# Optimization experiments

Measured on AMD Instinct MI355X. Metric: run time of the kernel, lower is better.

## Reference

```python
import jax, jax.numpy as jnp
import numpy as np

N = 50000      # nodes
E = 1600000    # edges (avg degree 32)
F_IN = 256     # input feature dim
H = 128        # hidden == output size of GCN
C = 40         # num_class


def setup_inputs() -> dict:
    key = jax.random.key(0)
    ks = jax.random.split(key, 13)
    inp = {
        "features": jax.random.normal(ks[0], (N, F_IN), dtype=jnp.float32),
        "src": jax.random.randint(ks[1], (E,), 0, N, dtype=jnp.int32),
        "dst": jax.random.randint(ks[2], (E,), 0, N, dtype=jnp.int32),
        "edge_weight": jax.random.uniform(ks[3], (E,), dtype=jnp.float32),
        "y": jax.random.normal(ks[4], (N, C), dtype=jnp.float32),
        # GCN layer 1
        "W1": jax.random.normal(ks[5], (F_IN, H), dtype=jnp.float32) / np.sqrt(F_IN),
        "b1": jnp.zeros((H,), dtype=jnp.float32),
        # GCN layer 2
        "W2": jax.random.normal(ks[6], (H, H), dtype=jnp.float32) / np.sqrt(H),
        "b2": jnp.zeros((H,), dtype=jnp.float32),
        # y_fc_emb: Linear(num_class, output_size)
        "We": jax.random.normal(ks[7], (C, H), dtype=jnp.float32) / np.sqrt(C),
        "be": jnp.zeros((H,), dtype=jnp.float32),
        # y_fc: Linear(hidden*2, num_class)
        "Wf": jax.random.normal(ks[8], (2 * H, C), dtype=jnp.float32) / np.sqrt(2 * H),
        "bf": jnp.zeros((C,), dtype=jnp.float32),
    }
    return inp


def _spmm(edge_weight, src, dst, x, n):
    # (sparse adj) @ x : out[i] = sum_{(j->i)} w_ji * x[j]
    return jax.ops.segment_sum(edge_weight[:, None] * x[src], dst, num_segments=n)


def reference(features, src, dst, edge_weight, y, W1, b1, W2, b2, We, be, Wf, bf):
    n = features.shape[0]
    # F.normalize: L2 row-normalize with eps=1e-12 clamp
    norm = jnp.maximum(jnp.linalg.norm(features, axis=1, keepdims=True), 1e-12)
    x = features / norm
    # GCN layer 1: relu(adj @ (x @ W1) + b1)   (dropout = 0)
    h = jax.nn.relu(_spmm(edge_weight, src, dst, x @ W1, n) + b1)
    # GCN layer 2: adj @ (h @ W2) + b2
    h = _spmm(edge_weight, src, dst, h @ W2, n) + b2
    # label embedding + head
    y_emb = y @ We + be
    logits = jnp.concatenate([y_emb, h], axis=1) @ Wf + bf
    return jax.nn.softmax(logits, axis=-1)
```

## Files before the change

### kernel.cpp

```cpp
#include <hip/hip_runtime.h>
#include <hip/hip_bf16.h>
#include <hip/hip_fp16.h>
#include <cstdint>
#include <cstddef>
#include <cmath>

#define F_IN 256
#define HDIM 128
#define CCLS 40
#define NBMAX 1024
#define EPB_H 16384

typedef short bf16x8 __attribute__((ext_vector_type(8)));
typedef float f32x4 __attribute__((ext_vector_type(4)));

__device__ inline unsigned pkbf(float a, float b) {
  __hip_bfloat162 h = __float22bfloat162_rn(make_float2(a, b));
  unsigned u;
  __builtin_memcpy(&u, &h, 4);
  return u;
}
__device__ inline unsigned short bfr(float f) {
  __hip_bfloat16 h = __float2bfloat16(f);
  unsigned short u;
  __builtin_memcpy(&u, &h, 2);
  return u;
}
__device__ inline float f16tof(unsigned short hb) {
  __half hv;
  __builtin_memcpy(&hv, &hb, 2);
  return __half2float(hv);
}
__device__ inline unsigned short ftof16(float f) {
  __half hv = __float2half(f);
  unsigned short u;
  __builtin_memcpy(&u, &hv, 2);
  return u;
}

__global__ __launch_bounds__(256) void prep_kernel(const float* __restrict__ x,
                                                   unsigned short* __restrict__ featbf,
                                                   const float* __restrict__ W1,
                                                   const float* __restrict__ W2,
                                                   unsigned short* __restrict__ W1T,
                                                   unsigned short* __restrict__ W2T,
                                                   const float* __restrict__ We,
                                                   const float* __restrict__ be,
                                                   const float* __restrict__ Wf,
                                                   const float* __restrict__ bf,
                                                   float* __restrict__ Wc,
                                                   float* __restrict__ bc,
                                                   const int* __restrict__ dst,
                                                   int* __restrict__ gcount,
                                                   int n, int e, int nb) {
  const int b = blockIdx.x;
  const int t = threadIdx.x;
  const int nblk = (n + 15) >> 4;
  if (b < nblk) {
    const int wv = t >> 6, l = t & 63;
    const int r0 = b * 16 + wv * 4;
    const bool q0 = r0 < n, q1 = r0 + 1 < n, q2 = r0 + 2 < n, q3 = r0 + 3 < n;
    const float* p = x + (size_t)r0 * F_IN + l * 4;
    float4 z = make_float4(0.f, 0.f, 0.f, 0.f);
    float4 v0 = q0 ? *(const float4*)(p) : z;
    float4 v1 = q1 ? *(const float4*)(p + F_IN) : z;
    float4 v2 = q2 ? *(const float4*)(p + 2 * F_IN) : z;
    float4 v3 = q3 ? *(const float4*)(p + 3 * F_IN) : z;
    float s0 = v0.x * v0.x + v0.y * v0.y + v0.z * v0.z + v0.w * v0.w;
    float s1 = v1.x * v1.x + v1.y * v1.y + v1.z * v1.z + v1.w * v1.w;
    float s2 = v2.x * v2.x + v2.y * v2.y + v2.z * v2.z + v2.w * v2.w;
    float s3 = v3.x * v3.x + v3.y * v3.y + v3.z * v3.z + v3.w * v3.w;
#pragma unroll
    for (int off = 32; off; off >>= 1) {
      s0 += __shfl_xor(s0, off, 64);
      s1 += __shfl_xor(s1, off, 64);
      s2 += __shfl_xor(s2, off, 64);
      s3 += __shfl_xor(s3, off, 64);
    }
    float i0 = 1.0f / fmaxf(sqrtf(s0), 1e-12f);
    float i1 = 1.0f / fmaxf(sqrtf(s1), 1e-12f);
    float i2 = 1.0f / fmaxf(sqrtf(s2), 1e-12f);
    float i3 = 1.0f / fmaxf(sqrtf(s3), 1e-12f);
    unsigned short* o = featbf + (size_t)r0 * F_IN + l * 4;
    if (q0) *(uint2*)(o) = make_uint2(pkbf(v0.x * i0, v0.y * i0), pkbf(v0.z * i0, v0.w * i0));
    if (q1) *(uint2*)(o + F_IN) = make_uint2(pkbf(v1.x * i1, v1.y * i1), pkbf(v1.z * i1, v1.w * i1));
    if (q2) *(uint2*)(o + 2 * F_IN) = make_uint2(pkbf(v2.x * i2, v2.y * i2), pkbf(v2.z * i2, v2.w * i2));
    if (q3) *(uint2*)(o + 3 * F_IN) = make_uint2(pkbf(v3.x * i3, v3.y * i3), pkbf(v3.z * i3, v3.w * i3));
  } else if (b < nblk + 192) {
    int idx = (b - nblk) * 256 + t;
    if (idx < 128 * 256) {
      int nr = idx >> 8, k = idx & 255;
      W1T[idx] = bfr(W1[k * 128 + nr]);
    } else {
      int i2 = idx - 128 * 256;
      if (i2 < 128 * 128) {
        int nr = i2 >> 7, k = i2 & 127;
        W2T[i2] = bfr(W2[k * 128 + nr]);
      }
    }
  } else if (b < nblk + 194) {
    int part = b - (nblk + 192);
    int lo = part * 800, hi = lo + 800;
    for (int i = lo + t; i < hi; i += 256) {
      int c = i / CCLS, j = i % CCLS;
      float s = 0.f;
      for (int f = 0; f < HDIM; ++f) s += We[c * HDIM + f] * Wf[f * CCLS + j];
      Wc[i] = s;
    }
    if (part == 0 && t < CCLS) {
      float s = bf[t];
      for (int f = 0; f < HDIM; ++f) s += be[f] * Wf[f * CCLS + t];
      bc[t] = s;
    }
  } else {
    __shared__ int h[NBMAX];
    for (int i = t; i < nb; i += 256) h[i] = 0;
    __syncthreads();
    int b4 = (b - (nblk + 194)) * (EPB_H / 4);
#pragma unroll
    for (int k = 0; k < EPB_H / 1024; ++k) {
      int gi = b4 + k * 256 + t;
      int e0 = gi * 4;
      int4 d = make_int4(-1, -1, -1, -1);
      if (e0 + 3 < e) d = ((const int4*)dst)[gi];
      else if (e0 < e) {
        d.x = dst[e0];
        if (e0 + 1 < e) d.y = dst[e0 + 1];
        if (e0 + 2 < e) d.z = dst[e0 + 2];
      }
      if (d.x >= 0) atomicAdd(&h[d.x >> 6], 1);
      if (d.y >= 0) atomicAdd(&h[d.y >> 6], 1);
      if (d.z >= 0) atomicAdd(&h[d.z >> 6], 1);
      if (d.w >= 0) atomicAdd(&h[d.w >> 6], 1);
    }
    __syncthreads();
    for (int i = t; i < nb; i += 256)
      if (h[i]) atomicAdd(&gcount[i], h[i]);
  }
}

__global__ __launch_bounds__(256) void bucket_scan(const int* __restrict__ gcount,
                                                   int* __restrict__ boff,
                                                   int* __restrict__ gcursor,
                                                   int* __restrict__ row_off,
                                                   int nb, int n) {
  __shared__ int part[256];
  int t = threadIdx.x;
  int v[4];
  int s = 0;
#pragma unroll
  for (int k = 0; k < 4; ++k) {
    int i = t * 4 + k;
    v[k] = (i < nb) ? gcount[i] : 0;
    s += v[k];
  }
  part[t] = s;
  __syncthreads();
  for (int off = 1; off < 256; off <<= 1) {
    int x = part[t];
    if (t >= off) x += part[t - off];
    __syncthreads();
    part[t] = x;
    __syncthreads();
  }
  int run = (t == 0) ? 0 : part[t - 1];
#pragma unroll
  for (int k = 0; k < 4; ++k) {
    int i = t * 4 + k;
    if (i < nb) { boff[i] = run; gcursor[i] = run; }
    run += v[k];
  }
  if (t == 255) { boff[nb] = part[255]; row_off[n] = part[255]; }
}

#define EPB 8192
__global__ __launch_bounds__(256) void bucket_scatter(const int* __restrict__ src,
                                                      const int* __restrict__ dst,
                                                      const float* __restrict__ w,
                                                      int* __restrict__ gcursor,
                                                      uint2* __restrict__ ews, int e, int nb) {
  __shared__ int hist[NBMAX];
  __shared__ int gbase[NBMAX];
  __shared__ int lcur[NBMAX];
  const int t = threadIdx.x;
  for (int i = t; i < nb; i += 256) { hist[i] = 0; lcur[i] = 0; }
  __syncthreads();
  const int b4 = blockIdx.x * 2048;
  int4 dv[8];
#pragma unroll
  for (int k = 0; k < 8; ++k) {
    int gi = b4 + k * 256 + t;
    int e0 = gi * 4;
    int4 d = make_int4(-1, -1, -1, -1);
    if (e0 + 3 < e) d = ((const int4*)dst)[gi];
    else if (e0 < e) {
      d.x = dst[e0];
      if (e0 + 1 < e) d.y = dst[e0 + 1];
      if (e0 + 2 < e) d.z = dst[e0 + 2];
    }
    dv[k] = d;
    if (d.x >= 0) atomicAdd(&hist[d.x >> 6], 1);
    if (d.y >= 0) atomicAdd(&hist[d.y >> 6], 1);
    if (d.z >= 0) atomicAdd(&hist[d.z >> 6], 1);
    if (d.w >= 0) atomicAdd(&hist[d.w >> 6], 1);
  }
  __syncthreads();
  for (int i = t; i < nb; i += 256) {
    int c = hist[i];
    gbase[i] = c ? atomicAdd(&gcursor[i], c) : 0;
  }
  __syncthreads();
#pragma unroll
  for (int k = 0; k < 8; ++k) {
    int gi = b4 + k * 256 + t;
    int e0 = gi * 4;
    if (e0 >= e) continue;
    int4 s4 = make_int4(0, 0, 0, 0);
    float4 w4 = make_float4(0.f, 0.f, 0.f, 0.f);
    if (e0 + 3 < e) { s4 = ((const int4*)src)[gi]; w4 = ((const float4*)w)[gi]; }
    else {
      s4.x = src[e0]; w4.x = w[e0];
      if (e0 + 1 < e) { s4.y = src[e0 + 1]; w4.y = w[e0 + 1]; }
      if (e0 + 2 < e) { s4.z = src[e0 + 2]; w4.z = w[e0 + 2]; }
    }
    int4 d = dv[k];
    if (d.x >= 0) { int bb = d.x >> 6; int r = atomicAdd(&lcur[bb], 1);
      ews[gbase[bb] + r] = make_uint2(((unsigned)(d.x & 63) << 26) | (unsigned)s4.x, __float_as_uint(w4.x)); }
    if (d.y >= 0) { int bb = d.y >> 6; int r = atomicAdd(&lcur[bb], 1);
      ews[gbase[bb] + r] = make_uint2(((unsigned)(d.y & 63) << 26) | (unsigned)s4.y, __float_as_uint(w4.y)); }
    if (d.z >= 0) { int bb = d.z >> 6; int r = atomicAdd(&lcur[bb], 1);
      ews[gbase[bb] + r] = make_uint2(((unsigned)(d.z & 63) << 26) | (unsigned)s4.z, __float_as_uint(w4.z)); }
    if (d.w >= 0) { int bb = d.w >> 6; int r = atomicAdd(&lcur[bb], 1);
      ews[gbase[bb] + r] = make_uint2(((unsigned)(d.w & 63) << 26) | (unsigned)s4.w, __float_as_uint(w4.w)); }
  }
}

__global__ __launch_bounds__(256) void bucket_sort(const uint2* __restrict__ ews,
                                                   const int* __restrict__ boff,
                                                   unsigned* __restrict__ ews2,
                                                   int* __restrict__ row_off,
                                                   int n) {
  __shared__ int cnt64[64];
  __shared__ int cur[64];
  const int t = threadIdx.x;
  const int b = blockIdx.x;
  const int e0 = boff[b], e1 = boff[b + 1];
  if (t < 64) cnt64[t] = 0;
  __syncthreads();
  for (int i = e0 + t; i < e1; i += 256) atomicAdd(&cnt64[(unsigned)ews[i].x >> 26], 1);
  __syncthreads();
  if (t == 0) {
    int run = 0;
    for (int d = 0; d < 64; ++d) {
      int c = cnt64[d];
      cur[d] = run;
      run += c;
    }
  }
  __syncthreads();
  if (t < 64) {
    int node = b * 64 + t;
    if (node < n) row_off[node] = e0 + cur[t];
  }
  __syncthreads();
  for (int i = e0 + t; i < e1; i += 256) {
    uint2 p = ews[i];
    int d = (unsigned)p.x >> 26;
    int pos = e0 + atomicAdd(&cur[d], 1);
    unsigned rec = (p.x & 0xFFFFu) | ((unsigned)ftof16(__uint_as_float(p.y)) << 16);
    ews2[pos] = rec;
  }
}

#define SPMM_PAIR(ua, ub)                                                      \
  {                                                                            \
    unsigned u = half ? (ub) : (ua);                                           \
    float wt = f16tof((unsigned short)(u >> 16));                              \
    const uint2 xv = *(const uint2*)(xin + (size_t)(u & 0xFFFFu) * HDIM + fo); \
    acc.x = fmaf(wt, __uint_as_float(xv.x << 16), acc.x);                      \
    acc.y = fmaf(wt, __uint_as_float(xv.x & 0xFFFF0000u), acc.y);              \
    acc.z = fmaf(wt, __uint_as_float(xv.y << 16), acc.z);                      \
    acc.w = fmaf(wt, __uint_as_float(xv.y & 0xFFFF0000u), acc.w);              \
  }

template <int OUT_BF16>
__global__ __launch_bounds__(256) void spmm_bf16(const unsigned short* __restrict__ xin,
                                                 const unsigned* __restrict__ ews,
                                                 const int* __restrict__ row_off,
                                                 const float* __restrict__ bias,
                                                 void* __restrict__ outp, int n,
                                                 int do_relu) {
  const int t = threadIdx.x;
  const int l = t & 63;
  const int node = blockIdx.x * 4 + (t >> 6);
  if (node >= n) return;
  const int ue0 = __builtin_amdgcn_readfirstlane(row_off[node]);
  const int ue1 = __builtin_amdgcn_readfirstlane(row_off[node + 1]);
  const int cnt = ue1 - ue0;
  const unsigned* ep = ews + ue0;
  const int fo = (l & 31) * 4;
  const int half = l >> 5;
  float4 acc = make_float4(0.f, 0.f, 0.f, 0.f);

  int k = 0;
  for (; k + 8 <= cnt; k += 8) {
    unsigned a0 = ep[k + 0], a1 = ep[k + 1], a2 = ep[k + 2], a3 = ep[k + 3];
    unsigned a4 = ep[k + 4], a5 = ep[k + 5], a6 = ep[k + 6], a7 = ep[k + 7];
    SPMM_PAIR(a0, a1);
    SPMM_PAIR(a2, a3);
    SPMM_PAIR(a4, a5);
    SPMM_PAIR(a6, a7);
  }
  for (; k < cnt; k += 2) {
    unsigned a0 = ep[k];
    unsigned a1 = (k + 1 < cnt) ? ep[k + 1] : 0u;
    SPMM_PAIR(a0, a1);
  }

  acc.x += __shfl_xor(acc.x, 32, 64);
  acc.y += __shfl_xor(acc.y, 32, 64);
  acc.z += __shfl_xor(acc.z, 32, 64);
  acc.w += __shfl_xor(acc.w, 32, 64);
  if (l < 32) {
    float4 bv = *(const float4*)(bias + fo);
    float4 r = make_float4(acc.x + bv.x, acc.y + bv.y, acc.z + bv.z, acc.w + bv.w);
    if (do_relu) {
      r.x = fmaxf(r.x, 0.f); r.y = fmaxf(r.y, 0.f);
      r.z = fmaxf(r.z, 0.f); r.w = fmaxf(r.w, 0.f);
    }
    if (OUT_BF16) {
      uint2 o = make_uint2(pkbf(r.x, r.y), pkbf(r.z, r.w));
      *(uint2*)((unsigned short*)outp + (size_t)node * HDIM + fo) = o;
    } else {
      *(float4*)((float*)outp + (size_t)node * HDIM + fo) = r;
    }
  }
}

template <int K>
__global__ __launch_bounds__(256) void gemm_mfma(const unsigned short* __restrict__ A,
                                                 const unsigned short* __restrict__ WT,
                                                 unsigned short* __restrict__ C, int M) {
  const int t = threadIdx.x;
  const int w = t >> 6, l = t & 63;
  const int ln = l & 15, quad = l >> 4;
  const int m0 = blockIdx.x * 64 + w * 16;
  const int arow = m0 + ln;
  const unsigned short* aptr = A + (size_t)(arow < M ? arow : (M - 1)) * K + quad * 8;

  f32x4 acc[8];
#pragma unroll
  for (int i = 0; i < 8; ++i) acc[i] = (f32x4){0.f, 0.f, 0.f, 0.f};

#pragma unroll
  for (int k0 = 0; k0 < K; k0 += 32) {
    bf16x8 af = *(const bf16x8*)(aptr + k0);
#pragma unroll
    for (int ti = 0; ti < 8; ++ti) {
      bf16x8 bf = *(const bf16x8*)(WT + (size_t)(ti * 16 + ln) * K + k0 + quad * 8);
      acc[ti] = __builtin_amdgcn_mfma_f32_16x16x32_bf16(af, bf, acc[ti], 0, 0, 0);
    }
  }

#pragma unroll
  for (int r = 0; r < 4; ++r) {
    int grow = m0 + quad * 4 + r;
    if (grow < M) {
      unsigned short* cp = C + (size_t)grow * HDIM + ln;
#pragma unroll
      for (int ti = 0; ti < 8; ++ti) cp[ti * 16] = bfr(acc[ti][r]);
    }
  }
}

__global__ __launch_bounds__(64) void head_kernel(const float* __restrict__ y,
                                                  const float* __restrict__ h2,
                                                  const float* __restrict__ Wc,
                                                  const float* __restrict__ bc,
                                                  const float* __restrict__ Wf,
                                                  float* __restrict__ out, int n) {
  __shared__ float sW[169 * CCLS];
  const int t = threadIdx.x;
  for (int i = t; i < 400; i += 64) ((float4*)sW)[i] = ((const float4*)Wc)[i];
  for (int i = t; i < 1280; i += 64)
    ((float4*)(sW + CCLS * CCLS))[i] = ((const float4*)(Wf + HDIM * CCLS))[i];
  if (t < 10) ((float4*)(sW + 168 * CCLS))[t] = ((const float4*)bc)[t];
  __syncthreads();

  const int node = blockIdx.x * 64 + t;
  const int nc = node < n ? node : n - 1;
  const float* zy = y + (size_t)nc * CCLS;
  const float* zh = h2 + (size_t)nc * HDIM;

  float acc[40];
#pragma unroll
  for (int cq = 0; cq < 10; ++cq) {
    float4 b4 = *(const float4*)&sW[168 * CCLS + cq * 4];
    acc[cq * 4 + 0] = b4.x; acc[cq * 4 + 1] = b4.y;
    acc[cq * 4 + 2] = b4.z; acc[cq * 4 + 3] = b4.w;
  }

#pragma unroll 2
  for (int kc = 0; kc < 10; ++kc) {
    float4 zv = *(const float4*)(zy + kc * 4);
    float zj[4] = {zv.x, zv.y, zv.z, zv.w};
#pragma unroll
    for (int j = 0; j < 4; ++j) {
      const float* wr = sW + (kc * 4 + j) * CCLS;
#pragma unroll
      for (int cq = 0; cq < 10; ++cq) {
        float4 w4 = *(const float4*)(wr + cq * 4);
        acc[cq * 4 + 0] = fmaf(zj[j], w4.x, acc[cq * 4 + 0]);
        acc[cq * 4 + 1] = fmaf(zj[j], w4.y, acc[cq * 4 + 1]);
        acc[cq * 4 + 2] = fmaf(zj[j], w4.z, acc[cq * 4 + 2]);
        acc[cq * 4 + 3] = fmaf(zj[j], w4.w, acc[cq * 4 + 3]);
      }
    }
  }
#pragma unroll 2
  for (int kc = 0; kc < 32; ++kc) {
    float4 zv = *(const float4*)(zh + kc * 4);
    float zj[4] = {zv.x, zv.y, zv.z, zv.w};
#pragma unroll
    for (int j = 0; j < 4; ++j) {
      const float* wr = sW + (40 + kc * 4 + j) * CCLS;
#pragma unroll
      for (int cq = 0; cq < 10; ++cq) {
        float4 w4 = *(const float4*)(wr + cq * 4);
        acc[cq * 4 + 0] = fmaf(zj[j], w4.x, acc[cq * 4 + 0]);
        acc[cq * 4 + 1] = fmaf(zj[j], w4.y, acc[cq * 4 + 1]);
        acc[cq * 4 + 2] = fmaf(zj[j], w4.z, acc[cq * 4 + 2]);
        acc[cq * 4 + 3] = fmaf(zj[j], w4.w, acc[cq * 4 + 3]);
      }
    }
  }

  float m = acc[0];
#pragma unroll
  for (int c = 1; c < 40; ++c) m = fmaxf(m, acc[c]);
  float sum = 0.f;
#pragma unroll
  for (int c = 0; c < 40; ++c) { acc[c] = __expf(acc[c] - m); sum += acc[c]; }
  float inv = 1.0f / sum;
  if (node < n) {
    float* op = out + (size_t)node * CCLS;
#pragma unroll
    for (int cq = 0; cq < 10; ++cq) {
      float4 o = make_float4(acc[cq * 4 + 0] * inv, acc[cq * 4 + 1] * inv,
                             acc[cq * 4 + 2] * inv, acc[cq * 4 + 3] * inv);
      *(float4*)(op + cq * 4) = o;
    }
  }
}

extern "C" void kernel_launch(void* const* d_in, const int* in_sizes, int n_in,
                              void* d_out, int out_size, void* d_ws, size_t ws_size,
                              hipStream_t stream) {
  (void)n_in; (void)out_size; (void)ws_size;
  const float* features = (const float*)d_in[0];
  const int*   src      = (const int*)d_in[1];
  const int*   dst      = (const int*)d_in[2];
  const float* ew       = (const float*)d_in[3];
  const float* y        = (const float*)d_in[4];
  const float* W1       = (const float*)d_in[5];
  const float* b1       = (const float*)d_in[6];
  const float* W2       = (const float*)d_in[7];
  const float* b2       = (const float*)d_in[8];
  const float* We       = (const float*)d_in[9];
  const float* be       = (const float*)d_in[10];
  const float* Wf       = (const float*)d_in[11];
  const float* bf       = (const float*)d_in[12];
  float* out = (float*)d_out;

  const int n = in_sizes[0] / F_IN;
  const int e = in_sizes[1];
  const int nb = (n + 63) >> 6;

  char* w = (char*)d_ws;
  auto take = [&](size_t bytes) {
    char* p = w;
    w += (bytes + 255) & ~(size_t)255;
    return p;
  };
  int*   gcount   = (int*)take((size_t)nb * 4);
  int*   boff     = (int*)take((size_t)(nb + 1) * 4);
  int*   gcursor  = (int*)take((size_t)nb * 4);
  int*   row_off  = (int*)take((size_t)(n + 1) * 4);
  uint2* ews      = (uint2*)take((size_t)e * 8);
  unsigned* ews2  = (unsigned*)take((size_t)(e + 16) * 4);
  unsigned short* featbf = (unsigned short*)take((size_t)n * F_IN * 2);
  unsigned short* bufH1  = (unsigned short*)take((size_t)n * HDIM * 2);
  unsigned short* bufH2  = (unsigned short*)take((size_t)n * HDIM * 2);
  float* bufS     = (float*)take((size_t)n * HDIM * 4);
  unsigned short* W1T = (unsigned short*)take((size_t)HDIM * F_IN * 2);
  unsigned short* W2T = (unsigned short*)take((size_t)HDIM * HDIM * 2);
  float* Wc       = (float*)take(CCLS * CCLS * 4);
  float* bc       = (float*)take(CCLS * 4);

  const int nblk = (n + 15) >> 4;
  const int hb = (e + EPB_H - 1) / EPB_H;
  hipMemsetAsync(gcount, 0, (size_t)nb * 4, stream);
  prep_kernel<<<nblk + 194 + hb, 256, 0, stream>>>(features, featbf, W1, W2, W1T, W2T,
                                                   We, be, Wf, bf, Wc, bc, dst, gcount,
                                                   n, e, nb);
  bucket_scan<<<1, 256, 0, stream>>>(gcount, boff, gcursor, row_off, nb, n);
  bucket_scatter<<<(e + EPB - 1) / EPB, 256, 0, stream>>>(src, dst, ew, gcursor, ews, e, nb);
  bucket_sort<<<nb, 256, 0, stream>>>(ews, boff, ews2, row_off, n);

  gemm_mfma<F_IN><<<(n + 63) / 64, 256, 0, stream>>>(featbf, W1T, bufH1, n);
  spmm_bf16<1><<<(n + 3) / 4, 256, 0, stream>>>(bufH1, ews2, row_off, b1, bufH2, n, 1);
  gemm_mfma<HDIM><<<(n + 63) / 64, 256, 0, stream>>>(bufH2, W2T, bufH1, n);
  spmm_bf16<0><<<(n + 3) / 4, 256, 0, stream>>>(bufH1, ews2, row_off, b2, bufS, n, 0);
  head_kernel<<<(n + 63) / 64, 64, 0, stream>>>(y, bufS, Wc, bc, Wf, out, n);
}
```

Measured before the change: 384.0 us.

## Split hidden features into column-chunk layout and run SpMM per chunk

Intermediate activations are stored in a chunked layout of 8 column blocks of 16 features ([chunk][node][16]). The SpMM runs eight blocks per node group, one per feature chunk, so each chunk's working set (50000 nodes × 32 bytes) is small enough to stay cache-resident while edges are gathered. The GEMM and head kernels are adapted to read and write this layout. The trade-off is that edge indices and weights are re-read eight times, and each gather becomes a 4-byte access with more shuffle reductions.

```diff
diff --git a/kernel.cpp b/kernel.cpp
--- a/kernel.cpp
+++ b/kernel.cpp
@@ -272,72 +272,66 @@
   }
 }
 
-#define SPMM_PAIR(ua, ub)                                                      \
-  {                                                                            \
-    unsigned u = half ? (ub) : (ua);                                           \
-    float wt = f16tof((unsigned short)(u >> 16));                              \
-    const uint2 xv = *(const uint2*)(xin + (size_t)(u & 0xFFFFu) * HDIM + fo); \
-    acc.x = fmaf(wt, __uint_as_float(xv.x << 16), acc.x);                      \
-    acc.y = fmaf(wt, __uint_as_float(xv.x & 0xFFFF0000u), acc.y);              \
-    acc.z = fmaf(wt, __uint_as_float(xv.y << 16), acc.z);                      \
-    acc.w = fmaf(wt, __uint_as_float(xv.y & 0xFFFF0000u), acc.w);              \
-  }
-
 template <int OUT_BF16>
-__global__ __launch_bounds__(256) void spmm_bf16(const unsigned short* __restrict__ xin,
-                                                 const unsigned* __restrict__ ews,
-                                                 const int* __restrict__ row_off,
-                                                 const float* __restrict__ bias,
-                                                 void* __restrict__ outp, int n,
-                                                 int do_relu) {
+__global__ __launch_bounds__(256) void spmm_chunk(const unsigned short* __restrict__ xin,
+                                                  const unsigned* __restrict__ ews,
+                                                  const int* __restrict__ row_off,
+                                                  const float* __restrict__ bias,
+                                                  void* __restrict__ outp, int n,
+                                                  int do_relu) {
   const int t = threadIdx.x;
   const int l = t & 63;
-  const int node = blockIdx.x * 4 + (t >> 6);
+  const int chunk = blockIdx.x & 7;
+  const int node = (blockIdx.x >> 3) * 4 + (t >> 6);
   if (node >= n) return;
   const int ue0 = __builtin_amdgcn_readfirstlane(row_off[node]);
   const int ue1 = __builtin_amdgcn_readfirstlane(row_off[node + 1]);
   const int cnt = ue1 - ue0;
   const unsigned* ep = ews + ue0;
-  const int fo = (l & 31) * 4;
-  const int half = l >> 5;
-  float4 acc = make_float4(0.f, 0.f, 0.f, 0.f);
-
+  const int g = l >> 3;
+  const int sub = l & 7;
+  const unsigned short* xc = xin + (size_t)chunk * n * 16 + sub * 2;
+  float ax = 0.f, ay = 0.f;
   int k = 0;
-  for (; k + 8 <= cnt; k += 8) {
-    unsigned a0 = ep[k + 0], a1 = ep[k + 1], a2 = ep[k + 2], a3 = ep[k + 3];
-    unsigned a4 = ep[k + 4], a5 = ep[k + 5], a6 = ep[k + 6], a7 = ep[k + 7];
-    SPMM_PAIR(a0, a1);
-    SPMM_PAIR(a2, a3);
-    SPMM_PAIR(a4, a5);
-    SPMM_PAIR(a6, a7);
-  }
-  for (; k < cnt; k += 2) {
-    unsigned a0 = ep[k];
-    unsigned a1 = (k + 1 < cnt) ? ep[k + 1] : 0u;
-    SPMM_PAIR(a0, a1);
-  }
-
-  acc.x += __shfl_xor(acc.x, 32, 64);
-  acc.y += __shfl_xor(acc.y, 32, 64);
-  acc.z += __shfl_xor(acc.z, 32, 64);
-  acc.w += __shfl_xor(acc.w, 32, 64);
-  if (l < 32) {
-    float4 bv = *(const float4*)(bias + fo);
-    float4 r = make_float4(acc.x + bv.x, acc.y + bv.y, acc.z + bv.z, acc.w + bv.w);
-    if (do_relu) {
-      r.x = fmaxf(r.x, 0.f); r.y = fmaxf(r.y, 0.f);
-      r.z = fmaxf(r.z, 0.f); r.w = fmaxf(r.w, 0.f);
-    }
+  for (; k + 16 <= cnt; k += 16) {
+    unsigned ra = ep[k + g];
+    unsigned rb = ep[k + 8 + g];
+    float wa = f16tof((unsigned short)(ra >> 16));
+    float wb = f16tof((unsigned short)(rb >> 16));
+    unsigned va = *(const unsigned*)(xc + (size_t)(ra & 0xFFFFu) * 16);
+    unsigned vb = *(const unsigned*)(xc + (size_t)(rb & 0xFFFFu) * 16);
+    ax = fmaf(wa, __uint_as_float(va << 16), ax);
+    ay = fmaf(wa, __uint_as_float(va & 0xFFFF0000u), ay);
+    ax = fmaf(wb, __uint_as_float(vb << 16), ax);
+    ay = fmaf(wb, __uint_as_float(vb & 0xFFFF0000u), ay);
+  }
+  for (; k < cnt; k += 8) {
+    int idx = k + g;
+    unsigned r = (idx < cnt) ? ep[idx] : 0u;
+    float wv = f16tof((unsigned short)(r >> 16));
+    unsigned v = *(const unsigned*)(xc + (size_t)(r & 0xFFFFu) * 16);
+    ax = fmaf(wv, __uint_as_float(v << 16), ax);
+    ay = fmaf(wv, __uint_as_float(v & 0xFFFF0000u), ay);
+  }
+#pragma unroll
+  for (int off = 8; off < 64; off <<= 1) {
+    ax += __shfl_xor(ax, off, 64);
+    ay += __shfl_xor(ay, off, 64);
+  }
+  if (g == 0) {
+    float2 bv = *(const float2*)(bias + chunk * 16 + sub * 2);
+    float rx = ax + bv.x, ry = ay + bv.y;
+    if (do_relu) { rx = fmaxf(rx, 0.f); ry = fmaxf(ry, 0.f); }
     if (OUT_BF16) {
-      uint2 o = make_uint2(pkbf(r.x, r.y), pkbf(r.z, r.w));
-      *(uint2*)((unsigned short*)outp + (size_t)node * HDIM + fo) = o;
+      *(unsigned*)((unsigned short*)outp + ((size_t)chunk * n + node) * 16 + sub * 2) = pkbf(rx, ry);
     } else {
-      *(float4*)((float*)outp + (size_t)node * HDIM + fo) = r;
-    }
-  }
-}
-
-template <int K>
+      *(float2*)((float*)outp + ((size_t)chunk * n + node) * 16 + sub * 2) =
+          make_float2(rx, ry);
+    }
+  }
+}
+
+template <int K, int CHA>
 __global__ __launch_bounds__(256) void gemm_mfma(const unsigned short* __restrict__ A,
                                                  const unsigned short* __restrict__ WT,
                                                  unsigned short* __restrict__ C, int M) {
@@ -346,7 +340,7 @@
   const int ln = l & 15, quad = l >> 4;
   const int m0 = blockIdx.x * 64 + w * 16;
   const int arow = m0 + ln;
-  const unsigned short* aptr = A + (size_t)(arow < M ? arow : (M - 1)) * K + quad * 8;
+  const int ac = arow < M ? arow : (M - 1);
 
   f32x4 acc[8];
 #pragma unroll
@@ -354,7 +348,11 @@
 
 #pragma unroll
   for (int k0 = 0; k0 < K; k0 += 32) {
-    bf16x8 af = *(const bf16x8*)(aptr + k0);
+    const int col = k0 + quad * 8;
+    const unsigned short* ap =
+        CHA ? A + ((size_t)(col >> 4) * M + ac) * 16 + (col & 15)
+            : A + (size_t)ac * K + col;
+    bf16x8 af = *(const bf16x8*)ap;
 #pragma unroll
     for (int ti = 0; ti < 8; ++ti) {
       bf16x8 bf = *(const bf16x8*)(WT + (size_t)(ti * 16 + ln) * K + k0 + quad * 8);
@@ -366,9 +364,9 @@
   for (int r = 0; r < 4; ++r) {
     int grow = m0 + quad * 4 + r;
     if (grow < M) {
-      unsigned short* cp = C + (size_t)grow * HDIM + ln;
-#pragma unroll
-      for (int ti = 0; ti < 8; ++ti) cp[ti * 16] = bfr(acc[ti][r]);
+#pragma unroll
+      for (int ti = 0; ti < 8; ++ti)
+        C[((size_t)ti * M + grow) * 16 + ln] = bfr(acc[ti][r]);
     }
   }
 }
@@ -390,7 +388,7 @@
   const int node = blockIdx.x * 64 + t;
   const int nc = node < n ? node : n - 1;
   const float* zy = y + (size_t)nc * CCLS;
-  const float* zh = h2 + (size_t)nc * HDIM;
+  const float* zh = h2 + (size_t)nc * 16;
 
   float acc[40];
 #pragma unroll
@@ -419,7 +417,7 @@
   }
 #pragma unroll 2
   for (int kc = 0; kc < 32; ++kc) {
-    float4 zv = *(const float4*)(zh + kc * 4);
+    float4 zv = *(const float4*)(zh + (size_t)(kc >> 2) * n * 16 + (kc & 3) * 4);
     float zj[4] = {zv.x, zv.y, zv.z, zv.w};
 #pragma unroll
     for (int j = 0; j < 4; ++j) {
@@ -507,9 +505,10 @@
   bucket_scatter<<<(e + EPB - 1) / EPB, 256, 0, stream>>>(src, dst, ew, gcursor, ews, e, nb);
   bucket_sort<<<nb, 256, 0, stream>>>(ews, boff, ews2, row_off, n);
 
-  gemm_mfma<F_IN><<<(n + 63) / 64, 256, 0, stream>>>(featbf, W1T, bufH1, n);
-  spmm_bf16<1><<<(n + 3) / 4, 256, 0, stream>>>(bufH1, ews2, row_off, b1, bufH2, n, 1);
-  gemm_mfma<HDIM><<<(n + 63) / 64, 256, 0, stream>>>(bufH2, W2T, bufH1, n);
-  spmm_bf16<0><<<(n + 3) / 4, 256, 0, stream>>>(bufH1, ews2, row_off, b2, bufS, n, 0);
+  const int nodeBlocks = (n + 3) / 4;
+  gemm_mfma<F_IN, 0><<<(n + 63) / 64, 256, 0, stream>>>(featbf, W1T, bufH1, n);
+  spmm_chunk<1><<<nodeBlocks * 8, 256, 0, stream>>>(bufH1, ews2, row_off, b1, bufH2, n, 1);
+  gemm_mfma<HDIM, 1><<<(n + 63) / 64, 256, 0, stream>>>(bufH2, W2T, bufH1, n);
+  spmm_chunk<0><<<nodeBlocks * 8, 256, 0, stream>>>(bufH1, ews2, row_off, b2, bufS, n, 0);
   head_kernel<<<(n + 63) / 64, 64, 0, stream>>>(y, bufS, Wc, bc, Wf, out, n);
 }
```

Result: slower. 530.3 us (+38.1%).
